# Kernel tuning notes

Hardware: AMD Instinct MI355X
Metric: run time of the kernel (lower is better)

The kernel has to match this reference:

```python
import jax, jax.numpy as jnp
import numpy as np

# Module constants (from init_kwargs): 2D domain, m=[1024,1024], omega=[0,1,0,1]
PAD = 2
M0, M1 = 1024, 1024
OMEGA_LO = np.array([0.0, 0.0], dtype=np.float32)   # omega[0::2]
H = np.array([1.0 / 1024.0, 1.0 / 1024.0], dtype=np.float32)  # (omega_hi-omega_lo)/m
N_POINTS = 2097152


def _b0(j, xi):
    # Cubic B-spline basis pieces, exactly as SplineInter.b0
    if j == 1:
        return (2 + xi) * (2 + xi) * (2 + xi)
    elif j == 2:
        return -(3 * xi + 6) * (xi * xi) + 4
    elif j == 3:
        return (3 * xi - 6) * (xi * xi) + 4
    elif j == 4:
        return (2 - xi) * (2 - xi) * (2 - xi)


def _basis(t):
    # t: [N] fractional part; returns [N,4] weights for offsets j=-1,0,1,2
    # matches b0(3 - j, t - j)
    return jnp.stack([_b0(3 - j, t - j) for j in range(-1, 3)], axis=-1)


def setup_inputs() -> dict:
    key = jax.random.key(0)
    k1, k2 = jax.random.split(key)
    # query points in physical domain [0,1)^2 -> normalized coords in [-0.5, 1023.5)
    x = jax.random.uniform(k1, (N_POINTS, 2), dtype=jnp.float32)
    # padded spline coefficient grid: (M0+2*PAD, M1+2*PAD)
    coeffs = 0.1 * jax.random.normal(k2, (M0 + 2 * PAD, M1 + 2 * PAD), dtype=jnp.float32)
    return {"x": x, "coeffs": coeffs}


def reference(x, coeffs):
    x = x.reshape(-1, 2)
    # normalize to grid coords
    xn = (x - jnp.asarray(OMEGA_LO)) / jnp.asarray(H) - 0.5  # [N,2]
    m = jnp.array([M0, M1], dtype=xn.dtype)
    valid = jnp.all((xn > -2) & (xn < m), axis=1)            # [N]
    P = jnp.floor(xn).astype(jnp.int32)                      # [N,2]
    t = xn - P                                               # fractional part [N,2]

    i1 = M1 + 2 * PAD  # row stride of padded coeff grid
    p = i1 * (PAD + P[:, 0]) + (PAD + P[:, 1])               # [N] base flat index

    w0 = _basis(t[:, 0])  # [N,4]
    w1 = _basis(t[:, 1])  # [N,4]

    js = jnp.arange(-1, 3, dtype=jnp.int32)
    idx = p[:, None, None] + js[:, None] * i1 + js[None, :]  # [N,4,4]
    cflat = coeffs.reshape(-1)
    safe_idx = jnp.clip(idx, 0, cflat.shape[0] - 1)
    vals = cflat[safe_idx]                                   # [N,4,4] gathered stencil

    out = jnp.einsum('nij,ni,nj->n', vals, w0, w1)
    out = jnp.where(valid, out, 0.0)
    return out[:, None]  # [N,1]
```

## Files before the change

kernel.cpp:

```cpp
#include <hip/hip_runtime.h>


#define I1 1028
#define TOTAL (1028 * 1028)

typedef float f4u __attribute__((ext_vector_type(4), aligned(4)));

__device__ __forceinline__ void basis4(float t, float w[4]) {
    float a = 1.0f - t;
    w[0] = a * a * a;
    w[1] = (3.0f * t - 6.0f) * (t * t) + 4.0f;
    float xi = t - 1.0f;
    w[2] = -(3.0f * xi + 6.0f) * (xi * xi) + 4.0f;
    w[3] = t * t * t;
}

__global__ __launch_bounds__(256) void spline_interp_kernel(
    const float* __restrict__ x,
    const float* __restrict__ coeffs,
    float* __restrict__ out,
    int n)
{
    int i = blockIdx.x * blockDim.x + threadIdx.x;
    if (i >= n) return;

    float2 xy = reinterpret_cast<const float2*>(x)[i];

    float xn0 = xy.x * 1024.0f - 0.5f;
    float xn1 = xy.y * 1024.0f - 0.5f;

    bool valid = (xn0 > -2.0f) && (xn0 < 1024.0f) &&
                 (xn1 > -2.0f) && (xn1 < 1024.0f);

    float P0f = floorf(xn0);
    float P1f = floorf(xn1);
    int P0 = (int)P0f;
    int P1 = (int)P1f;
    float t0 = xn0 - P0f;
    float t1 = xn1 - P1f;

    float w0[4], w1[4];
    basis4(t0, w0);
    basis4(t1, w1);

    int base = I1 * (2 + P0) + (2 + P1);

    bool interior = (base - I1 - 1 >= 0) && (base + 2 * I1 + 2 <= TOTAL - 1);

    float acc = 0.0f;
    if (interior) {
#pragma unroll
        for (int j = 0; j < 4; ++j) {
            int r = base + (j - 1) * I1 - 1;
            f4u v = *reinterpret_cast<const f4u*>(coeffs + r);
            float s = fmaf(v.x, w1[0],
                      fmaf(v.y, w1[1],
                      fmaf(v.z, w1[2],
                           v.w * w1[3])));
            acc = fmaf(s, w0[j], acc);
        }
    } else {
#pragma unroll
        for (int j = 0; j < 4; ++j) {
            int r = base + (j - 1) * I1 - 1;
            float s = 0.0f;
#pragma unroll
            for (int k = 0; k < 4; ++k) {
                int idx = r + k;
                idx = min(max(idx, 0), TOTAL - 1);
                s = fmaf(coeffs[idx], w1[k], s);
            }
            acc = fmaf(s, w0[j], acc);
        }
    }

    out[i] = valid ? acc : 0.0f;
}

extern "C" void kernel_launch(void* const* d_in, const int* in_sizes, int n_in,
                              void* d_out, int out_size, void* d_ws, size_t ws_size,
                              hipStream_t stream) {
    const float* x = (const float*)d_in[0];
    const float* coeffs = (const float*)d_in[1];
    float* out = (float*)d_out;

    int n = in_sizes[0] / 2;
    int block = 256;
    int grid = (n + block - 1) / block;
    spline_interp_kernel<<<grid, block, 0, stream>>>(x, coeffs, out, n);
}
```

Baseline: 110.4 us.

## Bin query points by grid tile and evaluate from shared-memory coefficient patches

Adds a counting sort of query points into 16x16 spatial tiles (histogram, scan, scatter kernels) and an eval kernel that stages each tile's 68x68 coefficient patch in LDS before evaluating that tile's points. The aim is to replace scattered global/cache gathers of the coefficient stencil with LDS reads. In exchange it adds several extra full passes over the point data, atomics, a workspace memset, and scattered writes of the outputs through the saved index. It falls back to the direct kernel if the workspace is too small.

```diff
diff --git a/kernel.cpp b/kernel.cpp
--- a/kernel.cpp
+++ b/kernel.cpp
@@ -3,6 +3,13 @@
 
 #define I1 1028
 #define TOTAL (1028 * 1028)
+#define NPTS_TILE 64
+#define NTILE_SIDE 16
+#define NTILES 256
+#define PATCH 68
+#define PATCH_STRIDE 69
+#define BPT 4
+#define SORT_BLOCKS 256
 
 typedef float f4u __attribute__((ext_vector_type(4), aligned(4)));
 
@@ -15,65 +22,198 @@
     w[3] = t * t * t;
 }
 
-__global__ __launch_bounds__(256) void spline_interp_kernel(
-    const float* __restrict__ x,
-    const float* __restrict__ coeffs,
-    float* __restrict__ out,
-    int n)
+__device__ __forceinline__ void point_cell(float2 xy, int& P0, int& P1,
+                                           float& t0, float& t1, bool& valid) {
+    float xn0 = xy.x * 1024.0f - 0.5f;
+    float xn1 = xy.y * 1024.0f - 0.5f;
+    valid = (xn0 > -2.0f) && (xn0 < 1024.0f) &&
+            (xn1 > -2.0f) && (xn1 < 1024.0f);
+    float P0f = floorf(xn0);
+    float P1f = floorf(xn1);
+    P0 = (int)P0f;
+    P1 = (int)P1f;
+    t0 = xn0 - P0f;
+    t1 = xn1 - P1f;
+}
+
+__device__ __forceinline__ int tile_of(int P0, int P1) {
+    int ty = min(max(P0, 0), 1023) >> 6;
+    int tx = min(max(P1, 0), 1023) >> 6;
+    return ty * NTILE_SIDE + tx;
+}
+
+__device__ __forceinline__ float eval_slow(const float* __restrict__ coeffs,
+                                           int base, const float w0[4],
+                                           const float w1[4]) {
+    float acc = 0.0f;
+#pragma unroll
+    for (int j = 0; j < 4; ++j) {
+        int r = base + (j - 1) * I1 - 1;
+        float s = 0.0f;
+#pragma unroll
+        for (int k = 0; k < 4; ++k) {
+            int idx = min(max(r + k, 0), TOTAL - 1);
+            s = fmaf(coeffs[idx], w1[k], s);
+        }
+        acc = fmaf(s, w0[j], acc);
+    }
+    return acc;
+}
+
+
+__global__ __launch_bounds__(256) void hist_kernel(
+    const float2* __restrict__ x2, int* __restrict__ hist, int n)
+{
+    __shared__ int h[NTILES];
+    h[threadIdx.x] = 0;
+    __syncthreads();
+    int stride = gridDim.x * blockDim.x;
+    for (int p = blockIdx.x * blockDim.x + threadIdx.x; p < n; p += stride) {
+        int P0, P1; float t0, t1; bool valid;
+        point_cell(x2[p], P0, P1, t0, t1, valid);
+        atomicAdd(&h[tile_of(P0, P1)], 1);
+    }
+    __syncthreads();
+    atomicAdd(&hist[threadIdx.x], h[threadIdx.x]);
+}
+
+__global__ __launch_bounds__(256) void scan_kernel(
+    const int* __restrict__ hist, int* __restrict__ offsets,
+    int* __restrict__ cursor, int n)
+{
+    __shared__ int h[NTILES];
+    int t = threadIdx.x;
+    h[t] = hist[t];
+    __syncthreads();
+    if (t == 0) {
+        int acc = 0;
+        for (int i = 0; i < NTILES; ++i) { int c = h[i]; h[i] = acc; acc += c; }
+    }
+    __syncthreads();
+    offsets[t] = h[t];
+    cursor[t] = h[t];
+    if (t == 0) offsets[NTILES] = n;
+}
+
+__global__ __launch_bounds__(256) void scatter_kernel(
+    const float2* __restrict__ x2, int* __restrict__ cursor,
+    float2* __restrict__ sxy, int* __restrict__ sidx, int n)
+{
+    __shared__ int h[NTILES];
+    __shared__ int base[NTILES];
+    int t = threadIdx.x;
+    int chunk = (n + gridDim.x - 1) / gridDim.x;
+    int lo = blockIdx.x * chunk;
+    int hi = min(n, lo + chunk);
+
+    h[t] = 0;
+    __syncthreads();
+    for (int p = lo + t; p < hi; p += blockDim.x) {
+        int P0, P1; float t0, t1; bool valid;
+        point_cell(x2[p], P0, P1, t0, t1, valid);
+        atomicAdd(&h[tile_of(P0, P1)], 1);
+    }
+    __syncthreads();
+    base[t] = atomicAdd(&cursor[t], h[t]);
+    h[t] = 0;
+    __syncthreads();
+    for (int p = lo + t; p < hi; p += blockDim.x) {
+        float2 xy = x2[p];
+        int P0, P1; float t0, t1; bool valid;
+        point_cell(xy, P0, P1, t0, t1, valid);
+        int tile = tile_of(P0, P1);
+        int r = atomicAdd(&h[tile], 1);
+        int pos = base[tile] + r;
+        sxy[pos] = xy;
+        sidx[pos] = p;
+    }
+}
+
+
+__global__ __launch_bounds__(256) void eval_kernel(
+    const float2* __restrict__ sxy, const int* __restrict__ sidx,
+    const int* __restrict__ offsets, const float* __restrict__ coeffs,
+    float* __restrict__ out)
+{
+    __shared__ float s_tile[PATCH * PATCH_STRIDE];
+
+    int tile = blockIdx.x / BPT;
+    int chunk = blockIdx.x % BPT;
+    int ty = tile / NTILE_SIDE;
+    int tx = tile % NTILE_SIDE;
+    int row0 = ty * NPTS_TILE;
+    int col0 = tx * NPTS_TILE;
+
+    for (int i = threadIdx.x; i < PATCH * PATCH; i += blockDim.x) {
+        int r = i / PATCH;
+        int c = i - r * PATCH;
+        s_tile[r * PATCH_STRIDE + c] = coeffs[(row0 + r) * I1 + (col0 + c)];
+    }
+    __syncthreads();
+
+    int seg_lo = offsets[tile];
+    int seg_hi = offsets[tile + 1];
+
+    for (int p = seg_lo + chunk * 256 + (int)threadIdx.x; p < seg_hi;
+         p += BPT * 256) {
+        float2 xy = sxy[p];
+        int P0, P1; float t0, t1; bool valid;
+        point_cell(xy, P0, P1, t0, t1, valid);
+
+        float w0[4], w1[4];
+        basis4(t0, w0);
+        basis4(t1, w1);
+
+        int lr = P0 + 1 - row0;
+        int lc = P1 + 1 - col0;
+
+        float acc;
+        if (lr >= 0 && lr <= 64 && lc >= 0 && lc <= 64) {
+            acc = 0.0f;
+#pragma unroll
+            for (int j = 0; j < 4; ++j) {
+                const float* row = &s_tile[(lr + j) * PATCH_STRIDE + lc];
+                float s = fmaf(row[0], w1[0],
+                          fmaf(row[1], w1[1],
+                          fmaf(row[2], w1[2],
+                               row[3] * w1[3])));
+                acc = fmaf(s, w0[j], acc);
+            }
+        } else {
+            int base = I1 * (2 + P0) + (2 + P1);
+            acc = eval_slow(coeffs, base, w0, w1);
+        }
+        out[sidx[p]] = valid ? acc : 0.0f;
+    }
+}
+
+
+__global__ __launch_bounds__(256) void spline_direct_kernel(
+    const float* __restrict__ x, const float* __restrict__ coeffs,
+    float* __restrict__ out, int n)
 {
     int i = blockIdx.x * blockDim.x + threadIdx.x;
     if (i >= n) return;
-
     float2 xy = reinterpret_cast<const float2*>(x)[i];
-
-    float xn0 = xy.x * 1024.0f - 0.5f;
-    float xn1 = xy.y * 1024.0f - 0.5f;
-
-    bool valid = (xn0 > -2.0f) && (xn0 < 1024.0f) &&
-                 (xn1 > -2.0f) && (xn1 < 1024.0f);
-
-    float P0f = floorf(xn0);
-    float P1f = floorf(xn1);
-    int P0 = (int)P0f;
-    int P1 = (int)P1f;
-    float t0 = xn0 - P0f;
-    float t1 = xn1 - P1f;
-
+    int P0, P1; float t0, t1; bool valid;
+    point_cell(xy, P0, P1, t0, t1, valid);
     float w0[4], w1[4];
     basis4(t0, w0);
     basis4(t1, w1);
-
     int base = I1 * (2 + P0) + (2 + P1);
-
     bool interior = (base - I1 - 1 >= 0) && (base + 2 * I1 + 2 <= TOTAL - 1);
-
     float acc = 0.0f;
     if (interior) {
 #pragma unroll
         for (int j = 0; j < 4; ++j) {
-            int r = base + (j - 1) * I1 - 1;
-            f4u v = *reinterpret_cast<const f4u*>(coeffs + r);
-            float s = fmaf(v.x, w1[0],
-                      fmaf(v.y, w1[1],
-                      fmaf(v.z, w1[2],
-                           v.w * w1[3])));
+            f4u v = *reinterpret_cast<const f4u*>(coeffs + base + (j - 1) * I1 - 1);
+            float s = fmaf(v.x, w1[0], fmaf(v.y, w1[1],
+                      fmaf(v.z, w1[2], v.w * w1[3])));
             acc = fmaf(s, w0[j], acc);
         }
     } else {
-#pragma unroll
-        for (int j = 0; j < 4; ++j) {
-            int r = base + (j - 1) * I1 - 1;
-            float s = 0.0f;
-#pragma unroll
-            for (int k = 0; k < 4; ++k) {
-                int idx = r + k;
-                idx = min(max(idx, 0), TOTAL - 1);
-                s = fmaf(coeffs[idx], w1[k], s);
-            }
-            acc = fmaf(s, w0[j], acc);
-        }
-    }
-
+        acc = eval_slow(coeffs, base, w0, w1);
+    }
     out[i] = valid ? acc : 0.0f;
 }
 
@@ -83,9 +223,28 @@
     const float* x = (const float*)d_in[0];
     const float* coeffs = (const float*)d_in[1];
     float* out = (float*)d_out;
-
     int n = in_sizes[0] / 2;
-    int block = 256;
-    int grid = (n + block - 1) / block;
-    spline_interp_kernel<<<grid, block, 0, stream>>>(x, coeffs, out, n);
-}
+
+    size_t need = 4096 + (size_t)n * 12;
+    if (ws_size < need) {
+        int block = 256;
+        int grid = (n + block - 1) / block;
+        spline_direct_kernel<<<grid, block, 0, stream>>>(x, coeffs, out, n);
+        return;
+    }
+
+    char* ws = (char*)d_ws;
+    int* hist    = (int*)(ws);
+    int* offsets = (int*)(ws + 1024);
+    int* cursor  = (int*)(ws + 2560);
+    float2* sxy  = (float2*)(ws + 4096);
+    int* sidx    = (int*)(ws + 4096 + (size_t)n * 8);
+
+    const float2* x2 = (const float2*)x;
+
+    hipMemsetAsync(d_ws, 0, 4096, stream);
+    hist_kernel<<<SORT_BLOCKS, 256, 0, stream>>>(x2, hist, n);
+    scan_kernel<<<1, 256, 0, stream>>>(hist, offsets, cursor, n);
+    scatter_kernel<<<SORT_BLOCKS, 256, 0, stream>>>(x2, cursor, sxy, sidx, n);
+    eval_kernel<<<NTILES * BPT, 256, 0, stream>>>(sxy, sidx, offsets, coeffs, out);
+}
```

New measurement: 136.6 us. 1.24x slower.

## Precompute fp16 per-cell 4x4 stencil table and gather one 32-byte record per point

Applied to the files above, without the earlier changes.

Adds a prep kernel that expands the coefficient grid into a per-cell table holding each cell's full 4x4 stencil as 16 fp16 values (32 bytes). The evaluation kernel then fetches one contiguous record per point instead of four row loads spread across the grid. This trades a 32 MB table build on every call for fewer, more contiguous gathers. Storing coefficients in fp16 lowers precision and could exceed the tolerance. If the workspace is too small, the old direct kernel is used.

```diff
diff --git a/kernel.cpp b/kernel.cpp
--- a/kernel.cpp
+++ b/kernel.cpp
@@ -5,6 +5,12 @@
 #define TOTAL (1028 * 1028)
 
 typedef float f4u __attribute__((ext_vector_type(4), aligned(4)));
+typedef _Float16 h16v __attribute__((ext_vector_type(16)));
+
+#define PREP_ROWS 16
+#define PREP_COLS 64
+#define PREP_SROWS (PREP_ROWS + 3)
+#define PREP_SCOLS (PREP_COLS + 3)
 
 __device__ __forceinline__ void basis4(float t, float w[4]) {
     float a = 1.0f - t;
@@ -15,65 +21,137 @@
     w[3] = t * t * t;
 }
 
-__global__ __launch_bounds__(256) void spline_interp_kernel(
-    const float* __restrict__ x,
-    const float* __restrict__ coeffs,
-    float* __restrict__ out,
-    int n)
+__device__ __forceinline__ void point_cell(float2 xy, int& P0, int& P1,
+                                           float& t0, float& t1, bool& valid) {
+    float xn0 = xy.x * 1024.0f - 0.5f;
+    float xn1 = xy.y * 1024.0f - 0.5f;
+    valid = (xn0 > -2.0f) && (xn0 < 1024.0f) &&
+            (xn1 > -2.0f) && (xn1 < 1024.0f);
+    float P0f = floorf(xn0);
+    float P1f = floorf(xn1);
+    P0 = (int)P0f;
+    P1 = (int)P1f;
+    t0 = xn0 - P0f;
+    t1 = xn1 - P1f;
+}
+
+__device__ __forceinline__ float eval_slow(const float* __restrict__ coeffs,
+                                           int base, const float w0[4],
+                                           const float w1[4]) {
+    float acc = 0.0f;
+#pragma unroll
+    for (int j = 0; j < 4; ++j) {
+        int r = base + (j - 1) * I1 - 1;
+        float s = 0.0f;
+#pragma unroll
+        for (int k = 0; k < 4; ++k) {
+            int idx = min(max(r + k, 0), TOTAL - 1);
+            s = fmaf(coeffs[idx], w1[k], s);
+        }
+        acc = fmaf(s, w0[j], acc);
+    }
+    return acc;
+}
+
+
+__global__ __launch_bounds__(256) void prep_kernel(
+    const float* __restrict__ coeffs, h16v* __restrict__ fat)
+{
+    __shared__ float s[PREP_SROWS * PREP_SCOLS];
+
+    int tile_x = blockIdx.x & 15;
+    int tile_y = blockIdx.x >> 4;
+    int r0 = tile_y * PREP_ROWS;
+    int c0 = tile_x * PREP_COLS;
+    int t = threadIdx.x;
+
+    for (int i = t; i < PREP_SROWS * PREP_SCOLS; i += 256) {
+        int rr = i / PREP_SCOLS;
+        int cc = i - rr * PREP_SCOLS;
+        s[i] = coeffs[(r0 + 1 + rr) * I1 + (c0 + 1 + cc)];
+    }
+    __syncthreads();
+
+#pragma unroll
+    for (int ii = 0; ii < (PREP_ROWS * PREP_COLS) / 256; ++ii) {
+        int l = ii * 256 + t;
+        int lr = l >> 6;
+        int lc = l & 63;
+        h16v v;
+#pragma unroll
+        for (int j = 0; j < 4; ++j) {
+#pragma unroll
+            for (int k = 0; k < 4; ++k) {
+                v[j * 4 + k] = (_Float16)s[(lr + j) * PREP_SCOLS + (lc + k)];
+            }
+        }
+        fat[(size_t)(r0 + lr) * 1024 + (c0 + lc)] = v;
+    }
+}
+
+
+__global__ __launch_bounds__(256) void fat_eval_kernel(
+    const float* __restrict__ x, const h16v* __restrict__ fat,
+    const float* __restrict__ coeffs, float* __restrict__ out, int n)
 {
     int i = blockIdx.x * blockDim.x + threadIdx.x;
     if (i >= n) return;
 
     float2 xy = reinterpret_cast<const float2*>(x)[i];
-
-    float xn0 = xy.x * 1024.0f - 0.5f;
-    float xn1 = xy.y * 1024.0f - 0.5f;
-
-    bool valid = (xn0 > -2.0f) && (xn0 < 1024.0f) &&
-                 (xn1 > -2.0f) && (xn1 < 1024.0f);
-
-    float P0f = floorf(xn0);
-    float P1f = floorf(xn1);
-    int P0 = (int)P0f;
-    int P1 = (int)P1f;
-    float t0 = xn0 - P0f;
-    float t1 = xn1 - P1f;
+    int P0, P1; float t0, t1; bool valid;
+    point_cell(xy, P0, P1, t0, t1, valid);
 
     float w0[4], w1[4];
     basis4(t0, w0);
     basis4(t1, w1);
 
+    float acc = 0.0f;
+    if (valid) {
+        if (P0 >= 0 && P1 >= 0) {
+            h16v v = fat[(size_t)P0 * 1024 + P1];
+#pragma unroll
+            for (int j = 0; j < 4; ++j) {
+                float s = fmaf((float)v[j * 4 + 0], w1[0],
+                          fmaf((float)v[j * 4 + 1], w1[1],
+                          fmaf((float)v[j * 4 + 2], w1[2],
+                               (float)v[j * 4 + 3] * w1[3])));
+                acc = fmaf(s, w0[j], acc);
+            }
+        } else {
+            int base = I1 * (2 + P0) + (2 + P1);
+            acc = eval_slow(coeffs, base, w0, w1);
+        }
+    }
+    out[i] = valid ? acc : 0.0f;
+}
+
+
+__global__ __launch_bounds__(256) void spline_direct_kernel(
+    const float* __restrict__ x, const float* __restrict__ coeffs,
+    float* __restrict__ out, int n)
+{
+    int i = blockIdx.x * blockDim.x + threadIdx.x;
+    if (i >= n) return;
+    float2 xy = reinterpret_cast<const float2*>(x)[i];
+    int P0, P1; float t0, t1; bool valid;
+    point_cell(xy, P0, P1, t0, t1, valid);
+    float w0[4], w1[4];
+    basis4(t0, w0);
+    basis4(t1, w1);
     int base = I1 * (2 + P0) + (2 + P1);
-
     bool interior = (base - I1 - 1 >= 0) && (base + 2 * I1 + 2 <= TOTAL - 1);
-
     float acc = 0.0f;
     if (interior) {
 #pragma unroll
         for (int j = 0; j < 4; ++j) {
-            int r = base + (j - 1) * I1 - 1;
-            f4u v = *reinterpret_cast<const f4u*>(coeffs + r);
-            float s = fmaf(v.x, w1[0],
-                      fmaf(v.y, w1[1],
-                      fmaf(v.z, w1[2],
-                           v.w * w1[3])));
+            f4u v = *reinterpret_cast<const f4u*>(coeffs + base + (j - 1) * I1 - 1);
+            float s = fmaf(v.x, w1[0], fmaf(v.y, w1[1],
+                      fmaf(v.z, w1[2], v.w * w1[3])));
             acc = fmaf(s, w0[j], acc);
         }
     } else {
-#pragma unroll
-        for (int j = 0; j < 4; ++j) {
-            int r = base + (j - 1) * I1 - 1;
-            float s = 0.0f;
-#pragma unroll
-            for (int k = 0; k < 4; ++k) {
-                int idx = r + k;
-                idx = min(max(idx, 0), TOTAL - 1);
-                s = fmaf(coeffs[idx], w1[k], s);
-            }
-            acc = fmaf(s, w0[j], acc);
-        }
+        acc = eval_slow(coeffs, base, w0, w1);
     }
-
     out[i] = valid ? acc : 0.0f;
 }
 
@@ -83,9 +161,22 @@
     const float* x = (const float*)d_in[0];
     const float* coeffs = (const float*)d_in[1];
     float* out = (float*)d_out;
+    int n = in_sizes[0] / 2;
 
-    int n = in_sizes[0] / 2;
+    size_t need = (size_t)1024 * 1024 * 32;
+    if (ws_size < need) {
+        int block = 256;
+        int grid = (n + block - 1) / block;
+        spline_direct_kernel<<<grid, block, 0, stream>>>(x, coeffs, out, n);
+        return;
+    }
+
+    h16v* fat = (h16v*)d_ws;
+
+    prep_kernel<<<(1024 / PREP_ROWS) * (1024 / PREP_COLS), 256, 0, stream>>>(
+        coeffs, fat);
+
     int block = 256;
     int grid = (n + block - 1) / block;
-    spline_interp_kernel<<<grid, block, 0, stream>>>(x, coeffs, out, n);
+    fat_eval_kernel<<<grid, block, 0, stream>>>(x, fat, coeffs, out, n);
 }
```

Result: no change. 110.9 us (+0.5%).
